# Performance work log

Measured on AMD Instinct MI355X. Metric: run time of the kernel, lower is better.

Reference implementation:

```python
import jax, jax.numpy as jnp
import numpy as np

B, C, H, W = 16, 256, 96, 96
P = 16          # num_prototypes
G = 8           # GroupNorm groups
EPS = 1e-5


def setup_inputs() -> dict:
    key = jax.random.key(0)
    ks = jax.random.split(key, 18)
    n = jax.random.normal
    return {
        "x": n(ks[0], (B, C, H, W), jnp.float32),
        "prototypes": n(ks[1], (1, P, C), jnp.float32),
        "pos_embed": n(ks[2], (1, C, 64, 64), jnp.float32) * 0.02,
        "q_w": n(ks[3], (C, C), jnp.float32) * (C ** -0.5),
        "q_b": n(ks[4], (C,), jnp.float32) * 0.01,
        "k_w": n(ks[5], (C, C), jnp.float32) * (C ** -0.5),
        "k_b": n(ks[6], (C,), jnp.float32) * 0.01,
        "v_w": n(ks[7], (C, C), jnp.float32) * (C ** -0.5),
        "v_b": n(ks[8], (C,), jnp.float32) * 0.01,
        "out_w": n(ks[9], (C, C), jnp.float32) * (C ** -0.5),
        "out_b": n(ks[10], (C,), jnp.float32) * 0.01,
        "dw_w": n(ks[11], (C, 1, 3, 3), jnp.float32) * (1.0 / 3.0),  # depthwise 3x3, no bias
        "bn_g": 1.0 + 0.1 * n(ks[12], (C,), jnp.float32),
        "bn_b": 0.1 * n(ks[13], (C,), jnp.float32),
        "bn_mean": 0.05 * n(ks[14], (C,), jnp.float32),
        "bn_var": 0.5 + jax.random.uniform(ks[15], (C,), jnp.float32),
        "gn_g": 1.0 + 0.1 * n(ks[16], (C,), jnp.float32),
        "gn_b": 0.1 * n(ks[17], (C,), jnp.float32),
    }


def _forward(x, prototypes, pos_embed, q_w, q_b, k_w, k_b, v_w, v_b,
             out_w, out_b, dw_w, bn_g, bn_b, bn_mean, bn_var, gn_g, gn_b):
    b, c, h, w = x.shape
    residual = x

    # bilinear interpolation of learnable PE (half-pixel centers == align_corners=False)
    pos = jax.image.resize(pos_embed, (1, c, h, w), method="bilinear")
    xp = x + pos

    # 1x1 conv Q projection -> [B, HW, C]
    q = jnp.einsum("bchw,dc->bhwd", xp, q_w) + q_b          # [B,H,W,C]
    q = q.reshape(b, h * w, c)

    # K/V from tiny prototype set (shared across batch) -> [P, C]
    k = prototypes[0] @ k_w.T + k_b
    v = prototypes[0] @ v_w.T + v_b

    # attention over only P=16 keys
    scale = c ** (-0.5)
    attn = jax.nn.softmax(jnp.einsum("bnc,pc->bnp", q, k) * scale, axis=-1)
    out = jnp.einsum("bnp,pc->bnc", attn, v)                # [B,HW,C]
    out = out.reshape(b, h, w, c).transpose(0, 3, 1, 2)     # [B,C,H,W]

    # 1x1 conv out projection
    out = jnp.einsum("bchw,dc->bdhw", out, out_w) + out_b[None, :, None, None]

    # local branch: depthwise 3x3 conv -> BN (eval, running stats) -> GELU(exact)
    dw = jax.lax.conv_general_dilated(
        out, dw_w, window_strides=(1, 1), padding="SAME",
        feature_group_count=c, dimension_numbers=("NCHW", "OIHW", "NCHW"))
    inv = (bn_g / jnp.sqrt(bn_var + EPS))[None, :, None, None]
    bn = (dw - bn_mean[None, :, None, None]) * inv + bn_b[None, :, None, None]
    out = out + jax.nn.gelu(bn, approximate=False)

    # GroupNorm(8, C) over residual sum
    y = out + residual
    yg = y.reshape(b, G, c // G, h, w)
    mu = yg.mean(axis=(2, 3, 4), keepdims=True)
    var = yg.var(axis=(2, 3, 4), keepdims=True)
    yn = ((yg - mu) * jax.lax.rsqrt(var + EPS)).reshape(b, c, h, w)
    return yn * gn_g[None, :, None, None] + gn_b[None, :, None, None]


def reference(x, prototypes, pos_embed, q_w, q_b, k_w, k_b, v_w, v_b,
              out_w, out_b, dw_w, bn_g, bn_b, bn_mean, bn_var, gn_g, gn_b):
    return _forward(x, prototypes, pos_embed, q_w, q_b, k_w, k_b, v_w, v_b,
                    out_w, out_b, dw_w, bn_g, bn_b, bn_mean, bn_var, gn_g, gn_b)
```

## Files before the change

### kernel.cpp

```cpp
#include <hip/hip_runtime.h>
#include <math.h>

#define C_   256
#define B_   16
#define HW_  9216
#define W_   96
#define H_   96
#define P_   16
#define EPS_ 1e-5f

typedef unsigned int u32;

__global__ __launch_bounds__(256) void k_kv(
    const float* __restrict__ proto, const float* __restrict__ kw,
    const float* __restrict__ kb, const float* __restrict__ vw,
    const float* __restrict__ vb, float* __restrict__ wk, float* __restrict__ wv,
    float* __restrict__ sums)
{
    __shared__ float pr[C_];
    const int p = blockIdx.x, d = threadIdx.x;
    if (p == 0) sums[d] = 0.f;
    pr[d] = proto[p * C_ + d];
    __syncthreads();
    float kk = kb[d], vv = vb[d];
    const float* kr = kw + d * C_;
    const float* vr = vw + d * C_;
    #pragma unroll 8
    for (int c = 0; c < C_; ++c) {
        const float pc = pr[c];
        kk = fmaf(pc, kr[c], kk);
        vv = fmaf(pc, vr[c], vv);
    }
    wk[p * C_ + d] = kk;
    wv[p * C_ + d] = vv;
}

__global__ __launch_bounds__(256) void k_mu(
    const float* __restrict__ wk, const float* __restrict__ wv,
    const float* __restrict__ qw, const float* __restrict__ qb,
    const float* __restrict__ ow,
    float* __restrict__ wm, float* __restrict__ wu, float* __restrict__ ws0)
{
    __shared__ float row[C_];
    __shared__ float red[C_];
    const int blk = blockIdx.x, t = threadIdx.x;
    if (blk < 16) {
        const int p = blk;
        row[t] = wk[p * C_ + t];
        __syncthreads();
        float mm = 0.f;
        #pragma unroll 8
        for (int d = 0; d < C_; ++d)
            mm = fmaf(row[d], qw[d * C_ + t], mm);
        wm[t * P_ + p] = mm;
        red[t] = qb[t] * row[t];
        __syncthreads();
        for (int s = 128; s > 0; s >>= 1) {
            if (t < s) red[t] += red[t + s];
            __syncthreads();
        }
        if (t == 0) ws0[p] = red[0];
    } else {
        const int p = blk - 16;
        row[t] = wv[p * C_ + t];
        __syncthreads();
        float uu = 0.f;
        const float* orow = ow + t * C_;
        #pragma unroll 8
        for (int c = 0; c < C_; ++c)
            uu = fmaf(row[c], orow[c], uu);
        wu[t * P_ + p] = uu;
    }
}

__global__ __launch_bounds__(256) void k_pd(
    const float* __restrict__ pos, const float* __restrict__ m,
    float* __restrict__ pd)
{
    const int n = blockIdx.x * 256 + threadIdx.x;
    const int h = n / W_, w = n - h * W_;
    float sy = (h + 0.5f) * (2.0f / 3.0f) - 0.5f;
    float sx = (w + 0.5f) * (2.0f / 3.0f) - 0.5f;
    sy = fminf(fmaxf(sy, 0.f), 63.f);
    sx = fminf(fmaxf(sx, 0.f), 63.f);
    const int y0 = (int)sy, x0 = (int)sx;
    const float fy = sy - (float)y0, fx = sx - (float)x0;
    const int y1 = min(y0 + 1, 63), x1 = min(x0 + 1, 63);
    const float w00 = (1.f - fy) * (1.f - fx), w01 = (1.f - fy) * fx;
    const float w10 = fy * (1.f - fx),         w11 = fy * fx;
    const int i00 = y0 * 64 + x0, i01 = y0 * 64 + x1;
    const int i10 = y1 * 64 + x0, i11 = y1 * 64 + x1;

    float acc[P_];
    #pragma unroll
    for (int p = 0; p < P_; ++p) acc[p] = 0.f;

    #pragma unroll 4
    for (int c = 0; c < C_; ++c) {
        const float* pc = pos + c * 4096;
        const float pv = pc[i00] * w00 + pc[i01] * w01 +
                         pc[i10] * w10 + pc[i11] * w11;
        #pragma unroll
        for (int p = 0; p < P_; ++p)
            acc[p] = fmaf(pv, m[c * P_ + p], acc[p]);
    }
    #pragma unroll
    for (int p = 0; p < P_; ++p) pd[p * HW_ + n] = acc[p];
}

__global__ __launch_bounds__(64) void k_logits(
    const float* __restrict__ x, const float* __restrict__ m,
    const float* __restrict__ s0, const float* __restrict__ pd,
    float* __restrict__ lw)
{
    const int n = blockIdx.x * 64 + threadIdx.x;
    const int b = n / HW_;
    const int npx = n - b * HW_;
    const float* xp = x + (size_t)b * (C_ * HW_) + npx;

    float acc[P_];
    #pragma unroll
    for (int p = 0; p < P_; ++p) acc[p] = 0.f;

    for (int cc = 0; cc < C_; cc += 16) {
        float xv[16];
        #pragma unroll
        for (int j = 0; j < 16; ++j)
            xv[j] = xp[(size_t)(cc + j) * HW_];
        #pragma unroll
        for (int j = 0; j < 16; ++j) {
            const float* mr = m + (cc + j) * P_;
            #pragma unroll
            for (int p = 0; p < P_; ++p)
                acc[p] = fmaf(xv[j], mr[p], acc[p]);
        }
    }

    float l[P_];
    float mx = -1e30f;
    #pragma unroll
    for (int p = 0; p < P_; ++p) {
        l[p] = (acc[p] + pd[(size_t)p * HW_ + npx] + s0[p]) * 0.0625f;
        mx = fmaxf(mx, l[p]);
    }
    float sum = 0.f;
    #pragma unroll
    for (int p = 0; p < P_; ++p) { l[p] = __expf(l[p] - mx); sum += l[p]; }
    const float r = 1.f / sum;

    float* lp = lw + (size_t)b * (P_ * HW_) + npx;
    #pragma unroll
    for (int p = 0; p < P_; ++p) lp[(size_t)p * HW_] = l[p] * r;
}

__global__ __launch_bounds__(256) void k_out(
    const float* __restrict__ lw, const float* __restrict__ u,
    const float* __restrict__ ob, float* __restrict__ o2)
{
    const int b = blockIdx.z;
    const int d0 = blockIdx.y * 8;
    const int px = blockIdx.x * 1024 + threadIdx.x * 4;

    const float* lp = lw + (size_t)b * (P_ * HW_) + px;
    float4 lv[P_];
    #pragma unroll
    for (int p = 0; p < P_; ++p)
        lv[p] = *reinterpret_cast<const float4*>(lp + (size_t)p * HW_);

    float* op = o2 + ((size_t)b * C_ + d0) * HW_ + px;
    #pragma unroll
    for (int j = 0; j < 8; ++j) {
        const int d = d0 + j;
        const float* ur = u + d * P_;
        const float obd = ob[d];
        float4 o = make_float4(obd, obd, obd, obd);
        #pragma unroll
        for (int p = 0; p < P_; ++p) {
            o.x = fmaf(lv[p].x, ur[p], o.x);
            o.y = fmaf(lv[p].y, ur[p], o.y);
            o.z = fmaf(lv[p].z, ur[p], o.z);
            o.w = fmaf(lv[p].w, ur[p], o.w);
        }
        *reinterpret_cast<float4*>(op + (size_t)j * HW_) = o;
    }
}

__global__ __launch_bounds__(256) void k_local(
    const float* __restrict__ x,
    const float* __restrict__ dww, const float* __restrict__ bng,
    const float* __restrict__ bnb, const float* __restrict__ bnm,
    const float* __restrict__ bnv,
    float* __restrict__ y, float* __restrict__ sums)
{
    __shared__ float tile[98 * 100];
    const int c = blockIdx.x, b = blockIdx.y, t = threadIdx.x;

    if (t < 100) { tile[t] = 0.f; tile[97 * 100 + t] = 0.f; }
    if (t < 96)  { tile[(t + 1) * 100 + 1] = 0.f; tile[(t + 1) * 100 + 98] = 0.f; }

    const size_t plane = (size_t)(b * C_ + c) * HW_;
    const float4* op4 = reinterpret_cast<const float4*>(y + plane);
    #pragma unroll
    for (int k = 0; k < 9; ++k) {
        const int g = t + k * 256;
        const int h = g / 24;
        const int w0 = (g - h * 24) * 4;
        const float4 v = op4[g];
        const int base = (h + 1) * 100 + w0 + 2;
        *reinterpret_cast<float2*>(&tile[base])     = make_float2(v.x, v.y);
        *reinterpret_cast<float2*>(&tile[base + 2]) = make_float2(v.z, v.w);
    }
    __syncthreads();

    const float w00 = dww[c * 9 + 0], w01 = dww[c * 9 + 1], w02 = dww[c * 9 + 2];
    const float w10 = dww[c * 9 + 3], w11 = dww[c * 9 + 4], w12 = dww[c * 9 + 5];
    const float w20 = dww[c * 9 + 6], w21 = dww[c * 9 + 7], w22 = dww[c * 9 + 8];
    const float inv  = bng[c] * rsqrtf(bnv[c] + EPS_);
    const float mu   = bnm[c];
    const float beta = bnb[c];

    const float4* xp4 = reinterpret_cast<const float4*>(x + plane);
    float4* yp4 = reinterpret_cast<float4*>(y + plane);
    float s1 = 0.f, s2 = 0.f;

    #pragma unroll
    for (int k = 0; k < 9; ++k) {
        const int g = t + k * 256;
        const float4 xv = xp4[g];
        const int h = g / 24;
        const int w0 = (g - h * 24) * 4;
        const int r0 = h * 100 + w0;
        const float4 a0 = *reinterpret_cast<const float4*>(&tile[r0]);
        const float4 a1 = *reinterpret_cast<const float4*>(&tile[r0 + 4]);
        const float4 b0 = *reinterpret_cast<const float4*>(&tile[r0 + 100]);
        const float4 b1 = *reinterpret_cast<const float4*>(&tile[r0 + 104]);
        const float4 c0 = *reinterpret_cast<const float4*>(&tile[r0 + 200]);
        const float4 c1 = *reinterpret_cast<const float4*>(&tile[r0 + 204]);
        const float A[8]  = {a0.x, a0.y, a0.z, a0.w, a1.x, a1.y, a1.z, a1.w};
        const float Bv[8] = {b0.x, b0.y, b0.z, b0.w, b1.x, b1.y, b1.z, b1.w};
        const float Cv[8] = {c0.x, c0.y, c0.z, c0.w, c1.x, c1.y, c1.z, c1.w};
        const float xs[4] = {xv.x, xv.y, xv.z, xv.w};
        float ys[4];
        #pragma unroll
        for (int j = 0; j < 4; ++j) {
            float dwv = A[j + 1] * w00 + A[j + 2] * w01 + A[j + 3] * w02
                      + Bv[j + 1] * w10 + Bv[j + 2] * w11 + Bv[j + 3] * w12
                      + Cv[j + 1] * w20 + Cv[j + 2] * w21 + Cv[j + 3] * w22;
            const float bn = (dwv - mu) * inv + beta;
            const float gl = 0.5f * bn * (1.f + erff(bn * 0.70710678118654752f));
            const float yv = Bv[j + 2] + gl + xs[j];
            s1 += yv;
            s2 = fmaf(yv, yv, s2);
            ys[j] = yv;
        }
        yp4[g] = make_float4(ys[0], ys[1], ys[2], ys[3]);
    }

    __syncthreads();
    float* red = tile;
    red[t] = s1; red[256 + t] = s2;
    __syncthreads();
    for (int s = 128; s > 0; s >>= 1) {
        if (t < s) { red[t] += red[t + s]; red[256 + t] += red[256 + t + s]; }
        __syncthreads();
    }
    if (t == 0) {
        const int bg = b * 8 + (c >> 5);
        atomicAdd(&sums[bg * 2 + 0], red[0]);
        atomicAdd(&sums[bg * 2 + 1], red[256]);
    }
}

__global__ __launch_bounds__(256) void k_norm(
    const float* __restrict__ sums, const float* __restrict__ gng,
    const float* __restrict__ gnb, float* __restrict__ y)
{
    const u32 i0 = ((u32)blockIdx.x * 256u + threadIdx.x) * 4u;
    const u32 plane = i0 / HW_;
    const u32 c = plane & 255u;
    const u32 b = plane >> 8;
    const u32 bg = b * 8u + (c >> 5);
    const float cntinv = 1.f / 294912.f;
    const float mean = sums[bg * 2 + 0] * cntinv;
    const float var  = fmaf(sums[bg * 2 + 1], cntinv, -mean * mean);
    const float inv  = rsqrtf(var + EPS_);
    const float a  = gng[c] * inv;
    const float bb = gnb[c] - mean * a;

    float4 v = *reinterpret_cast<const float4*>(y + i0);
    v.x = fmaf(v.x, a, bb);
    v.y = fmaf(v.y, a, bb);
    v.z = fmaf(v.z, a, bb);
    v.w = fmaf(v.w, a, bb);
    *reinterpret_cast<float4*>(y + i0) = v;
}

extern "C" void kernel_launch(void* const* d_in, const int* in_sizes, int n_in,
                              void* d_out, int out_size, void* d_ws, size_t ws_size,
                              hipStream_t stream)
{
    const float* x     = (const float*)d_in[0];
    const float* proto = (const float*)d_in[1];
    const float* pos   = (const float*)d_in[2];
    const float* qw    = (const float*)d_in[3];
    const float* qb    = (const float*)d_in[4];
    const float* kw    = (const float*)d_in[5];
    const float* kb    = (const float*)d_in[6];
    const float* vw    = (const float*)d_in[7];
    const float* vb    = (const float*)d_in[8];
    const float* ow    = (const float*)d_in[9];
    const float* ob    = (const float*)d_in[10];
    const float* dww   = (const float*)d_in[11];
    const float* bng   = (const float*)d_in[12];
    const float* bnb   = (const float*)d_in[13];
    const float* bnm   = (const float*)d_in[14];
    const float* bnv   = (const float*)d_in[15];
    const float* gng   = (const float*)d_in[16];
    const float* gnb   = (const float*)d_in[17];

    char* ws = (char*)d_ws;
    float* sums = (float*)(ws);
    float* s0   = (float*)(ws + 1024);
    float* wk   = (float*)(ws + 2048);
    float* wv   = (float*)(ws + 2048 + 16384);
    float* wm   = (float*)(ws + 2048 + 2 * 16384);
    float* wu   = (float*)(ws + 2048 + 3 * 16384);
    float* pd   = (float*)(ws + 2048 + 4 * 16384);
    float* lw   = (float*)(ws + 2048 + 4 * 16384 + 589824);

    float* out = (float*)d_out;

    k_kv<<<16, 256, 0, stream>>>(proto, kw, kb, vw, vb, wk, wv, sums);
    k_mu<<<32, 256, 0, stream>>>(wk, wv, qw, qb, ow, wm, wu, s0);
    k_pd<<<36, 256, 0, stream>>>(pos, wm, pd);
    k_logits<<<2304, 64, 0, stream>>>(x, wm, s0, pd, lw);
    k_out<<<dim3(9, 32, 16), 256, 0, stream>>>(lw, wu, ob, out);
    k_local<<<dim3(256, 16), 256, 0, stream>>>(x, dww, bng, bnb, bnm, bnv, out, sums);
    k_norm<<<36864, 256, 0, stream>>>(sums, gng, gnb, out);
}
```

Baseline: 528.6 us.

## Split depthwise-conv tiles into half planes, use fast erf approximation, separate output buffer

The local-branch kernel now handles half a plane per block (48 rows plus halo) using a z grid dimension. This halves shared memory per block and doubles the block count, aiming at better occupancy and latency hiding. Because the two halves share halo rows, the result is written to a separate workspace buffer instead of in place, and the norm kernel reads from that buffer and writes the final output. The exact erff GELU is replaced by an Abramowitz-Stegun polynomial with __expf, which is cheaper but less accurate (about 1e-7 absolute error in erf).

New measurement: 550.1 us. 1.04x slower.

```diff
diff --git a/kernel.cpp b/kernel.cpp
--- a/kernel.cpp
+++ b/kernel.cpp
@@ -10,6 +10,20 @@
 #define EPS_ 1e-5f
 
 typedef unsigned int u32;
+
+__device__ __forceinline__ float gelu_f(float v)
+{
+    const float z = fabsf(v) * 0.70710678118654752f;
+    const float t = 1.0f / fmaf(0.3275911f, z, 1.0f);
+    float poly = fmaf(1.061405429f, t, -1.453152027f);
+    poly = fmaf(poly, t, 1.421413741f);
+    poly = fmaf(poly, t, -0.284496736f);
+    poly = fmaf(poly, t, 0.254829592f);
+    poly *= t;
+    const float e = __expf(-z * z);
+    const float er = copysignf(1.0f - poly * e, v);
+    return 0.5f * v * (1.0f + er);
+}
 
 __global__ __launch_bounds__(256) void k_kv(
     const float* __restrict__ proto, const float* __restrict__ kw,
@@ -186,29 +200,33 @@
 }
 
 __global__ __launch_bounds__(256) void k_local(
-    const float* __restrict__ x,
+    const float* __restrict__ x, const float* __restrict__ o2,
     const float* __restrict__ dww, const float* __restrict__ bng,
     const float* __restrict__ bnb, const float* __restrict__ bnm,
     const float* __restrict__ bnv,
     float* __restrict__ y, float* __restrict__ sums)
 {
-    __shared__ float tile[98 * 100];
+    __shared__ float tile[50 * 100];
     const int c = blockIdx.x, b = blockIdx.y, t = threadIdx.x;
-
-    if (t < 100) { tile[t] = 0.f; tile[97 * 100 + t] = 0.f; }
-    if (t < 96)  { tile[(t + 1) * 100 + 1] = 0.f; tile[(t + 1) * 100 + 98] = 0.f; }
+    const int r0 = blockIdx.z * 48;
+
+    if (t < 50) { tile[t * 100 + 1] = 0.f; tile[t * 100 + 98] = 0.f; }
 
     const size_t plane = (size_t)(b * C_ + c) * HW_;
-    const float4* op4 = reinterpret_cast<const float4*>(y + plane);
-    #pragma unroll
-    for (int k = 0; k < 9; ++k) {
+    const float* o2p = o2 + plane;
+    #pragma unroll
+    for (int k = 0; k < 5; ++k) {
         const int g = t + k * 256;
-        const int h = g / 24;
-        const int w0 = (g - h * 24) * 4;
-        const float4 v = op4[g];
-        const int base = (h + 1) * 100 + w0 + 2;
-        *reinterpret_cast<float2*>(&tile[base])     = make_float2(v.x, v.y);
-        *reinterpret_cast<float2*>(&tile[base + 2]) = make_float2(v.z, v.w);
+        if (g < 1200) {
+            const int tr = g / 24, wq = g - tr * 24;
+            const int ir = r0 - 1 + tr;
+            float4 v = make_float4(0.f, 0.f, 0.f, 0.f);
+            if (ir >= 0 && ir <= 95)
+                v = *reinterpret_cast<const float4*>(o2p + ir * 96 + wq * 4);
+            const int base = tr * 100 + wq * 4 + 2;
+            *reinterpret_cast<float2*>(&tile[base])     = make_float2(v.x, v.y);
+            *reinterpret_cast<float2*>(&tile[base + 2]) = make_float2(v.z, v.w);
+        }
     }
     __syncthreads();
 
@@ -224,36 +242,38 @@
     float s1 = 0.f, s2 = 0.f;
 
     #pragma unroll
-    for (int k = 0; k < 9; ++k) {
+    for (int k = 0; k < 5; ++k) {
         const int g = t + k * 256;
-        const float4 xv = xp4[g];
-        const int h = g / 24;
-        const int w0 = (g - h * 24) * 4;
-        const int r0 = h * 100 + w0;
-        const float4 a0 = *reinterpret_cast<const float4*>(&tile[r0]);
-        const float4 a1 = *reinterpret_cast<const float4*>(&tile[r0 + 4]);
-        const float4 b0 = *reinterpret_cast<const float4*>(&tile[r0 + 100]);
-        const float4 b1 = *reinterpret_cast<const float4*>(&tile[r0 + 104]);
-        const float4 c0 = *reinterpret_cast<const float4*>(&tile[r0 + 200]);
-        const float4 c1 = *reinterpret_cast<const float4*>(&tile[r0 + 204]);
-        const float A[8]  = {a0.x, a0.y, a0.z, a0.w, a1.x, a1.y, a1.z, a1.w};
-        const float Bv[8] = {b0.x, b0.y, b0.z, b0.w, b1.x, b1.y, b1.z, b1.w};
-        const float Cv[8] = {c0.x, c0.y, c0.z, c0.w, c1.x, c1.y, c1.z, c1.w};
-        const float xs[4] = {xv.x, xv.y, xv.z, xv.w};
-        float ys[4];
-        #pragma unroll
-        for (int j = 0; j < 4; ++j) {
-            float dwv = A[j + 1] * w00 + A[j + 2] * w01 + A[j + 3] * w02
-                      + Bv[j + 1] * w10 + Bv[j + 2] * w11 + Bv[j + 3] * w12
-                      + Cv[j + 1] * w20 + Cv[j + 2] * w21 + Cv[j + 3] * w22;
-            const float bn = (dwv - mu) * inv + beta;
-            const float gl = 0.5f * bn * (1.f + erff(bn * 0.70710678118654752f));
-            const float yv = Bv[j + 2] + gl + xs[j];
-            s1 += yv;
-            s2 = fmaf(yv, yv, s2);
-            ys[j] = yv;
-        }
-        yp4[g] = make_float4(ys[0], ys[1], ys[2], ys[3]);
+        if (g < 1152) {
+            const int lr = g / 24, wq = g - lr * 24;
+            const int w0 = wq * 4;
+            const int gpx = (r0 + lr) * 24 + wq;
+            const float4 xv = xp4[gpx];
+            const int rb = lr * 100 + w0;
+            const float4 a0 = *reinterpret_cast<const float4*>(&tile[rb]);
+            const float4 a1 = *reinterpret_cast<const float4*>(&tile[rb + 4]);
+            const float4 b0 = *reinterpret_cast<const float4*>(&tile[rb + 100]);
+            const float4 b1 = *reinterpret_cast<const float4*>(&tile[rb + 104]);
+            const float4 c0 = *reinterpret_cast<const float4*>(&tile[rb + 200]);
+            const float4 c1 = *reinterpret_cast<const float4*>(&tile[rb + 204]);
+            const float A[8]  = {a0.x, a0.y, a0.z, a0.w, a1.x, a1.y, a1.z, a1.w};
+            const float Bv[8] = {b0.x, b0.y, b0.z, b0.w, b1.x, b1.y, b1.z, b1.w};
+            const float Cv[8] = {c0.x, c0.y, c0.z, c0.w, c1.x, c1.y, c1.z, c1.w};
+            const float xs[4] = {xv.x, xv.y, xv.z, xv.w};
+            float ys[4];
+            #pragma unroll
+            for (int j = 0; j < 4; ++j) {
+                float dwv = A[j + 1] * w00 + A[j + 2] * w01 + A[j + 3] * w02
+                          + Bv[j + 1] * w10 + Bv[j + 2] * w11 + Bv[j + 3] * w12
+                          + Cv[j + 1] * w20 + Cv[j + 2] * w21 + Cv[j + 3] * w22;
+                const float bn = (dwv - mu) * inv + beta;
+                const float yv = Bv[j + 2] + gelu_f(bn) + xs[j];
+                s1 += yv;
+                s2 = fmaf(yv, yv, s2);
+                ys[j] = yv;
+            }
+            yp4[gpx] = make_float4(ys[0], ys[1], ys[2], ys[3]);
+        }
     }
 
     __syncthreads();
@@ -273,7 +293,8 @@
 
 __global__ __launch_bounds__(256) void k_norm(
     const float* __restrict__ sums, const float* __restrict__ gng,
-    const float* __restrict__ gnb, float* __restrict__ y)
+    const float* __restrict__ gnb, const float* __restrict__ ysrc,
+    float* __restrict__ dst)
 {
     const u32 i0 = ((u32)blockIdx.x * 256u + threadIdx.x) * 4u;
     const u32 plane = i0 / HW_;
@@ -287,12 +308,12 @@
     const float a  = gng[c] * inv;
     const float bb = gnb[c] - mean * a;
 
-    float4 v = *reinterpret_cast<const float4*>(y + i0);
+    float4 v = *reinterpret_cast<const float4*>(ysrc + i0);
     v.x = fmaf(v.x, a, bb);
     v.y = fmaf(v.y, a, bb);
     v.z = fmaf(v.z, a, bb);
     v.w = fmaf(v.w, a, bb);
-    *reinterpret_cast<float4*>(y + i0) = v;
+    *reinterpret_cast<float4*>(dst + i0) = v;
 }
 
 extern "C" void kernel_launch(void* const* d_in, const int* in_sizes, int n_in,
@@ -327,6 +348,7 @@
     float* wu   = (float*)(ws + 2048 + 3 * 16384);
     float* pd   = (float*)(ws + 2048 + 4 * 16384);
     float* lw   = (float*)(ws + 2048 + 4 * 16384 + 589824);
+    float* yws  = (float*)(ws + (size_t)16777216);
 
     float* out = (float*)d_out;
 
@@ -335,6 +357,6 @@
     k_pd<<<36, 256, 0, stream>>>(pos, wm, pd);
     k_logits<<<2304, 64, 0, stream>>>(x, wm, s0, pd, lw);
     k_out<<<dim3(9, 32, 16), 256, 0, stream>>>(lw, wu, ob, out);
-    k_local<<<dim3(256, 16), 256, 0, stream>>>(x, dww, bng, bnb, bnm, bnv, out, sums);
-    k_norm<<<36864, 256, 0, stream>>>(sums, gng, gnb, out);
-}
+    k_local<<<dim3(256, 16, 2), 256, 0, stream>>>(x, out, dww, bng, bnb, bnm, bnv, yws, sums);
+    k_norm<<<36864, 256, 0, stream>>>(sums, gng, gnb, yws, out);
+}
```
